# Optimization experiments

Hardware: AMD Instinct MI355X
Metric: run time of the kernel (lower is better)

The kernel has to match this reference:

```python
import jax, jax.numpy as jnp
import numpy as np
import math

D_MODEL, N_HEADS, D_HEAD, D_MLP = 768, 12, 64, 3072
EPS = 1e-5
IGNORE = -100000.0


def _ln(x, w, b):
    mu = jnp.mean(x, axis=-1, keepdims=True)
    xc = x - mu
    scale = jnp.sqrt(jnp.mean(xc * xc, axis=-1, keepdims=True) + EPS)
    return (xc / scale) * w + b


def _gelu_new(x):
    # GPT-2 'new' gelu
    return 0.5 * x * (1.0 + jnp.tanh(jnp.sqrt(2.0 / jnp.pi) * (x + 0.044715 * x ** 3)))


def setup_inputs() -> dict:
    key = jax.random.key(0)
    ks = jax.random.split(key, 12)
    std = 0.02
    inp = {
        "resid_pre": jax.random.normal(ks[0], (8, 1024, D_MODEL), jnp.float32),
        "W_Q": jax.random.normal(ks[1], (N_HEADS, D_MODEL, D_HEAD), jnp.float32) * std,
        "b_Q": jnp.zeros((N_HEADS, D_HEAD), jnp.float32),
        "W_K": jax.random.normal(ks[2], (N_HEADS, D_MODEL, D_HEAD), jnp.float32) * std,
        "b_K": jnp.zeros((N_HEADS, D_HEAD), jnp.float32),
        "W_V": jax.random.normal(ks[3], (N_HEADS, D_MODEL, D_HEAD), jnp.float32) * std,
        "b_V": jnp.zeros((N_HEADS, D_HEAD), jnp.float32),
        "W_O": jax.random.normal(ks[4], (N_HEADS, D_HEAD, D_MODEL), jnp.float32) * std,
        "b_O": jnp.zeros((D_MODEL,), jnp.float32),
        "ln1_w": jnp.ones((D_MODEL,), jnp.float32),
        "ln1_b": jnp.zeros((D_MODEL,), jnp.float32),
        "ln2_w": jnp.ones((D_MODEL,), jnp.float32),
        "ln2_b": jnp.zeros((D_MODEL,), jnp.float32),
        "W_in": jax.random.normal(ks[5], (D_MODEL, D_MLP), jnp.float32) * std,
        "b_in": jnp.zeros((D_MLP,), jnp.float32),
        "W_out": jax.random.normal(ks[6], (D_MLP, D_MODEL), jnp.float32) * std,
        "b_out": jnp.zeros((D_MODEL,), jnp.float32),
    }
    return inp


def reference(resid_pre, W_Q, b_Q, W_K, b_K, W_V, b_V, W_O, b_O,
              ln1_w, ln1_b, ln2_w, ln2_b, W_in, b_in, W_out, b_out):
    # ---- ln1 + attention ----
    n = _ln(resid_pre, ln1_w, ln1_b)  # [b, s, d]; broadcast over heads in einsums
    q = jnp.einsum('bsd,hde->bshe', n, W_Q) + b_Q
    k = jnp.einsum('bsd,hde->bshe', n, W_K) + b_K
    v = jnp.einsum('bsd,hde->bshe', n, W_V) + b_V
    scores = jnp.einsum('bqhe,bkhe->bhqk', q, k) / math.sqrt(D_HEAD)
    S = scores.shape[-1]
    causal = jnp.triu(jnp.ones((S, S), dtype=bool), k=1)
    scores = jnp.where(causal, IGNORE, scores)
    pattern = jax.nn.softmax(scores, axis=-1)
    z = jnp.einsum('bhqk,bkhe->bqhe', pattern, v)
    # per-head output with b_O / n_heads each (as in source), then summed over heads
    attn_per_head = jnp.einsum('bqhe,hed->bqhd', z, W_O) + b_O / N_HEADS
    attn_out = attn_per_head.sum(axis=2)  # [b, s, d]
    resid_mid = resid_pre + attn_out
    # ---- ln2 + mlp ----
    n2 = _ln(resid_mid, ln2_w, ln2_b)
    pre = jnp.einsum('bsd,dm->bsm', n2, W_in) + b_in
    post = _gelu_new(pre)
    mlp_out = jnp.einsum('bsm,md->bsd', post, W_out) + b_out
    return resid_mid + mlp_out
```

## Files before the change

kernel.cpp:

```cpp
#include <hip/hip_runtime.h>
#include <hip/hip_bf16.h>

typedef unsigned short u16;
typedef float f32x4 __attribute__((ext_vector_type(4)));
typedef __bf16 bf16x8 __attribute__((ext_vector_type(8)));
typedef unsigned short u16x8 __attribute__((ext_vector_type(8)));
typedef unsigned short u16x4 __attribute__((ext_vector_type(4)));

__device__ __forceinline__ float b2f(u16 u) {
    unsigned v = ((unsigned)u) << 16;
    return __builtin_bit_cast(float, v);
}
__device__ __forceinline__ u16 f2b(float f) {
    unsigned u = __builtin_bit_cast(unsigned, f);
    u += 0x7fffu + ((u >> 16) & 1u);
    return (u16)(u >> 16);
}
__device__ __forceinline__ bf16x8 ldfrag(const u16* p) {
    return __builtin_bit_cast(bf16x8, *(const u16x8*)p);
}
__device__ __forceinline__ f32x4 mfma16(bf16x8 a, bf16x8 b, f32x4 c) {
    return __builtin_amdgcn_mfma_f32_16x16x32_bf16(a, b, c, 0, 0, 0);
}
__device__ __forceinline__ void gload_lds16(const u16* g, u16* l) {
    __builtin_amdgcn_global_load_lds(
        (const __attribute__((address_space(1))) unsigned int*)(g),
        (__attribute__((address_space(3))) unsigned int*)(l), 16, 0, 0);
}

#define T_TOK 8192
#define DM 768
#define NH 12
#define DH 64
#define DMLP 3072
#define SEQ 1024
#define QKV_LD 2304
#define QK_LD 1536

#define OFF_WQKV ((size_t)0)
#define OFF_WO   (OFF_WQKV + (size_t)2304*768)
#define OFF_WIN  (OFF_WO   + (size_t)768*768)
#define OFF_WOUT (OFF_WIN  + (size_t)768*3072)
#define OFF_BQKV (OFF_WOUT + (size_t)3072*768)
#define P0       (OFF_BQKV + (size_t)4608)

#define SZ_N    ((size_t)T_TOK*DM)
#define SZ_QKV  ((size_t)T_TOK*QKV_LD)
#define A_NBUF   (P0)
#define A_QKV    (P0 + SZ_N)
#define A_Z      (P0 + SZ_N + SZ_QKV)
#define A_N2     (P0)
#define A_POST   (P0 + SZ_N)
#define PATHA_BYTES (((size_t)(P0 + SZ_N + SZ_QKV + SZ_N)) * 2)
#define B_Z      (P0)
#define B_QKVB   (P0 + SZ_N)
#define B_NBUF   (B_QKVB + (size_t)SEQ*QKV_LD)
#define B_N2     (P0)
#define B_POSTC  (P0 + SZ_N)

#define PR0 (2304*768)
#define PR1 (768*768)
#define PR2 (768*3072)
#define PR3 (3072*768)
#define PREP_TOTAL (PR0+PR1+PR2+PR3+2304)

__global__ __launch_bounds__(256) void prep_kernel(
    const float* __restrict__ WQ, const float* __restrict__ WK, const float* __restrict__ WV,
    const float* __restrict__ WO, const float* __restrict__ Win, const float* __restrict__ Wout,
    const float* __restrict__ bQ, const float* __restrict__ bK, const float* __restrict__ bV,
    u16* __restrict__ Wqkv_t, u16* __restrict__ Wo_t, u16* __restrict__ Win_t,
    u16* __restrict__ Wout_t, float* __restrict__ bias_qkv)
{
    int idx = blockIdx.x * 256 + threadIdx.x;
    if (idx < PR0) {
        int r = idx / 768, d = idx % 768;
        int which = r / 768;
        int he = r % 768;
        int h = he >> 6, e = he & 63;
        const float* W = (which == 0) ? WQ : ((which == 1) ? WK : WV);
        Wqkv_t[idx] = f2b(W[h * 49152 + d * 64 + e]);
    } else if (idx < PR0 + PR1) {
        int o = idx - PR0;
        int d = o / 768, he = o % 768;
        Wo_t[o] = f2b(WO[he * 768 + d]);
    } else if (idx < PR0 + PR1 + PR2) {
        int o = idx - PR0 - PR1;
        int m = o / 768, d = o % 768;
        Win_t[o] = f2b(Win[d * 3072 + m]);
    } else if (idx < PR0 + PR1 + PR2 + PR3) {
        int o = idx - PR0 - PR1 - PR2;
        int d = o / 3072, m = o % 3072;
        Wout_t[o] = f2b(Wout[m * 768 + d]);
    } else if (idx < PREP_TOTAL) {
        int j = idx - (PR0 + PR1 + PR2 + PR3);
        bias_qkv[j] = (j < 768) ? bQ[j] : ((j < 1536) ? bK[j - 768] : bV[j - 1536]);
    }
}

__global__ __launch_bounds__(256) void ln_kernel(
    const float* __restrict__ x, const float* __restrict__ w,
    const float* __restrict__ bb, u16* __restrict__ out)
{
    __shared__ float red[4];
    size_t base = (size_t)blockIdx.x * DM;
    int tid = threadIdx.x;
    float v0 = x[base + tid], v1 = x[base + tid + 256], v2 = x[base + tid + 512];
    float s = v0 + v1 + v2;
#pragma unroll
    for (int off = 32; off > 0; off >>= 1) s += __shfl_xor(s, off);
    if ((tid & 63) == 0) red[tid >> 6] = s;
    __syncthreads();
    float mu = (red[0] + red[1] + red[2] + red[3]) * (1.0f / 768.0f);
    v0 -= mu; v1 -= mu; v2 -= mu;
    float q = v0 * v0 + v1 * v1 + v2 * v2;
    __syncthreads();
#pragma unroll
    for (int off = 32; off > 0; off >>= 1) q += __shfl_xor(q, off);
    if ((tid & 63) == 0) red[tid >> 6] = q;
    __syncthreads();
    float var = (red[0] + red[1] + red[2] + red[3]) * (1.0f / 768.0f);
    float sc = rsqrtf(var + 1e-5f);
    out[base + tid]       = f2b(v0 * sc * w[tid]       + bb[tid]);
    out[base + tid + 256] = f2b(v1 * sc * w[tid + 256] + bb[tid + 256]);
    out[base + tid + 512] = f2b(v2 * sc * w[tid + 512] + bb[tid + 512]);
}

template <int EPI, int TM>
__global__ __launch_bounds__(256) void gemm_bt_kernel(
    const u16* __restrict__ A, const u16* __restrict__ BT,
    const float* __restrict__ bias, const float* __restrict__ aux,
    void* __restrict__ outp, int N, int K)
{
    __shared__ __align__(16) u16 As[TM * 32];
    __shared__ __align__(16) u16 Bs[128 * 32];
    const int tid = threadIdx.x;
    const int w = tid >> 6, l = tid & 63;
    const int lr = l & 15, lq = l >> 4;
    const int bm = blockIdx.x * TM, bn = blockIdx.y * 128;
    constexpr int MT = TM / 32;
    const int wm = (w >> 1) * (TM / 2), wn = (w & 1) * 64;

    f32x4 acc[MT][4];
#pragma unroll
    for (int i = 0; i < MT; i++)
#pragma unroll
        for (int j = 0; j < 4; j++) acc[i][j] = f32x4{0.f, 0.f, 0.f, 0.f};

    const int srow_a = (TM == 128) ? (w * 32 + (l >> 2)) : (w * 16 + (l >> 2));
    const int srow_b = w * 32 + (l >> 2);
    const int scol = ((l & 3) ^ ((l >> 2) & 3)) * 8;
    const u16* Ab = A  + (size_t)(bm + srow_a) * K + scol;
    const u16* Bb = BT + (size_t)(bn + srow_b) * K + scol;
    u16* AsD = As + ((TM == 128) ? w * 1024 : w * 512);
    u16* BsD = Bs + w * 1024;
    const int rchunk = (lq ^ (lr & 3)) * 8;

    const int kiter = K >> 5;
    for (int kk = 0; kk < kiter; ++kk) {
        const int k0 = kk * 32;
        gload_lds16(Ab + k0, AsD);
        if (TM == 128) gload_lds16(Ab + 16 * K + k0, AsD + 512);
        gload_lds16(Bb + k0,          BsD);
        gload_lds16(Bb + 16 * K + k0, BsD + 512);
        __syncthreads();
        bf16x8 af[MT], bf[4];
#pragma unroll
        for (int mt = 0; mt < MT; mt++) af[mt] = ldfrag(&As[(wm + mt * 16 + lr) * 32 + rchunk]);
#pragma unroll
        for (int nt = 0; nt < 4; nt++) bf[nt] = ldfrag(&Bs[(wn + nt * 16 + lr) * 32 + rchunk]);
#pragma unroll
        for (int mt = 0; mt < MT; mt++)
#pragma unroll
            for (int nt = 0; nt < 4; nt++)
                acc[mt][nt] = mfma16(af[mt], bf[nt], acc[mt][nt]);
        __syncthreads();
    }

    if (EPI == 4) {
        const bool isv = (bn >= 1536);
        u16* vtg = (u16*)aux;
#pragma unroll
        for (int mt = 0; mt < MT; mt++) {
            int row0 = bm + wm + mt * 16 + lq * 4;
            if (!isv) {
#pragma unroll
                for (int r = 0; r < 4; r++) {
                    size_t ro = (size_t)(row0 + r) * QK_LD;
#pragma unroll
                    for (int nt = 0; nt < 4; nt++) {
                        int col = bn + wn + nt * 16 + lr;
                        ((u16*)outp)[ro + col] = f2b(acc[mt][nt][r] + bias[col]);
                    }
                }
            } else {
                int bloc = row0 >> 10;
                int s = row0 & 1023;
#pragma unroll
                for (int nt = 0; nt < 4; nt++) {
                    int col = bn + wn + nt * 16 + lr;
                    int he = col - 1536;
                    float bcol = bias[col];
                    u16x4 pk;
                    pk[0] = f2b(acc[mt][nt][0] + bcol);
                    pk[1] = f2b(acc[mt][nt][1] + bcol);
                    pk[2] = f2b(acc[mt][nt][2] + bcol);
                    pk[3] = f2b(acc[mt][nt][3] + bcol);
                    *(u16x4*)&vtg[(size_t)bloc * (NH * 64 * SEQ)
                                  + (size_t)he * SEQ + s] = pk;
                }
            }
        }
        return;
    }

#pragma unroll
    for (int mt = 0; mt < MT; mt++) {
#pragma unroll
        for (int r = 0; r < 4; r++) {
            int row = bm + wm + mt * 16 + lq * 4 + r;
            size_t ro = (size_t)row * N;
#pragma unroll
            for (int nt = 0; nt < 4; nt++) {
                int col = bn + wn + nt * 16 + lr;
                float v = acc[mt][nt][r] + bias[col];
                if (EPI == 0) {
                    ((u16*)outp)[ro + col] = f2b(v);
                } else if (EPI == 1) {
                    ((float*)outp)[ro + col] = v + aux[ro + col];
                } else if (EPI == 2) {
                    float x = v;
                    float y = 0.7978845608028654f * (x + 0.044715f * x * x * x);
                    ((u16*)outp)[ro + col] = f2b(x / (1.0f + __expf(-2.0f * y)));
                } else {
                    ((float*)outp)[ro + col] = v + aux[ro + col];
                }
            }
        }
    }
}

__global__ __launch_bounds__(256, 5) void attn_kernel(
    const u16* __restrict__ qk, const u16* __restrict__ vtg,
    u16* __restrict__ z, int b0, int bq0)
{
    __shared__ __align__(16) u16 Ks[64 * 72];
    __shared__ __align__(16) u16 Vt[64 * 72];
    __shared__ __align__(16) u16 Ps[4][16 * 72];

    const int qt = (int)(gridDim.x - 1) - (int)blockIdx.x;
    const int bh = blockIdx.y;
    const int b = b0 + bh / NH, h = bh % NH;
    const int tid = threadIdx.x, w = tid >> 6, l = tid & 63;
    const int lr = l & 15, lq = l >> 4;
    const int qbase = qt * 64;
    const u16* qp = qk + (size_t)(b - bq0) * SEQ * QK_LD + h * 64;
    const u16* kp = qp + 768;
    const u16* vthead = vtg + ((size_t)(b - bq0) * NH + h) * (64 * SEQ);
    u16* PsW = &Ps[w][0];

    bf16x8 aq0, aq1;
    {
        const u16* qrow = qp + (size_t)(qbase + w * 16 + lr) * QK_LD + lq * 8;
        aq0 = ldfrag(qrow);
        aq1 = ldfrag(qrow + 32);
    }

    float m_i = -1e30f;
    float l_i = 0.f;
    f32x4 O[4];
#pragma unroll
    for (int i = 0; i < 4; i++) O[i] = f32x4{0.f, 0.f, 0.f, 0.f};

    const int nkt = qt + 1;
    const int srow = tid >> 2;
    const int spart = (tid & 3) * 16;

    u16x8 kreg0, kreg1, vreg0, vreg1;
    {
        const u16* ks = kp + (size_t)srow * QK_LD + spart;
        kreg0 = *(const u16x8*)ks;
        kreg1 = *(const u16x8*)(ks + 8);
        const u16* vs = vthead + (size_t)srow * SEQ + spart;
        vreg0 = *(const u16x8*)vs;
        vreg1 = *(const u16x8*)(vs + 8);
    }

    for (int kt = 0; kt < nkt; ++kt) {
        __syncthreads();
        *(u16x8*)&Ks[srow * 72 + spart]     = kreg0;
        *(u16x8*)&Ks[srow * 72 + spart + 8] = kreg1;
        *(u16x8*)&Vt[srow * 72 + spart]     = vreg0;
        *(u16x8*)&Vt[srow * 72 + spart + 8] = vreg1;
        __syncthreads();
        if (kt + 1 < nkt) {
            const u16* ks = kp + (size_t)((kt + 1) * 64 + srow) * QK_LD + spart;
            kreg0 = *(const u16x8*)ks;
            kreg1 = *(const u16x8*)(ks + 8);
            const u16* vs = vthead + (size_t)srow * SEQ + (kt + 1) * 64 + spart;
            vreg0 = *(const u16x8*)vs;
            vreg1 = *(const u16x8*)(vs + 8);
        }

        f32x4 S[4];
#pragma unroll
        for (int nt = 0; nt < 4; nt++) S[nt] = f32x4{0.f, 0.f, 0.f, 0.f};
#pragma unroll
        for (int nt = 0; nt < 4; nt++) {
            bf16x8 bk0 = ldfrag(&Ks[(nt * 16 + lr) * 72 + lq * 8]);
            bf16x8 bk1 = ldfrag(&Ks[(nt * 16 + lr) * 72 + 32 + lq * 8]);
            S[nt] = mfma16(bk0, aq0, S[nt]);
            S[nt] = mfma16(bk1, aq1, S[nt]);
        }

        const bool diag = (kt == qt);
        float mx = -1e30f;
#pragma unroll
        for (int nt = 0; nt < 4; nt++)
#pragma unroll
            for (int r = 0; r < 4; r++) {
                float sv = S[nt][r] * 0.125f;
                if (diag) sv = (nt * 16 + lq * 4 + r <= w * 16 + lr) ? sv : -1e30f;
                S[nt][r] = sv;
                mx = fmaxf(mx, sv);
            }
        mx = fmaxf(mx, __shfl_xor(mx, 16));
        mx = fmaxf(mx, __shfl_xor(mx, 32));
        float mn = fmaxf(m_i, mx);
        float alpha = __expf(m_i - mn);
        m_i = mn;
        float rs = 0.f;
#pragma unroll
        for (int nt = 0; nt < 4; nt++) {
            u16x4 pk;
#pragma unroll
            for (int r = 0; r < 4; r++) {
                float pe = __expf(S[nt][r] - mn);
                rs += pe;
                pk[r] = f2b(pe);
            }
            *(u16x4*)&PsW[lr * 72 + nt * 16 + lq * 4] = pk;
        }
        rs += __shfl_xor(rs, 16);
        rs += __shfl_xor(rs, 32);
        l_i = l_i * alpha + rs;

#pragma unroll
        for (int r = 0; r < 4; r++) {
            float ar = __shfl(alpha, (l & 48) | (lq * 4 + r));
            O[0][r] *= ar; O[1][r] *= ar; O[2][r] *= ar; O[3][r] *= ar;
        }

#pragma unroll
        for (int kq = 0; kq < 2; kq++) {
            bf16x8 ap = ldfrag(&PsW[lr * 72 + kq * 32 + lq * 8]);
#pragma unroll
            for (int ot = 0; ot < 4; ot++) {
                bf16x8 bv = ldfrag(&Vt[(ot * 16 + lr) * 72 + kq * 32 + lq * 8]);
                O[ot] = mfma16(ap, bv, O[ot]);
            }
        }
    }

    float li[4];
#pragma unroll
    for (int r = 0; r < 4; r++)
        li[r] = __shfl(l_i, (l & 48) | (lq * 4 + r));
#pragma unroll
    for (int ot = 0; ot < 4; ot++)
#pragma unroll
        for (int r = 0; r < 4; r++) {
            int q = qbase + w * 16 + lq * 4 + r;
            size_t t = (size_t)b * SEQ + q;
            z[t * DM + h * 64 + ot * 16 + lr] = f2b(O[ot][r] / li[r]);
        }
}

extern "C" void kernel_launch(void* const* d_in, const int* in_sizes, int n_in,
                              void* d_out, int out_size, void* d_ws, size_t ws_size,
                              hipStream_t stream) {
    const float* resid_pre = (const float*)d_in[0];
    const float* W_Q  = (const float*)d_in[1];
    const float* b_Q  = (const float*)d_in[2];
    const float* W_K  = (const float*)d_in[3];
    const float* b_K  = (const float*)d_in[4];
    const float* W_V  = (const float*)d_in[5];
    const float* b_V  = (const float*)d_in[6];
    const float* W_O  = (const float*)d_in[7];
    const float* b_O  = (const float*)d_in[8];
    const float* ln1w = (const float*)d_in[9];
    const float* ln1b = (const float*)d_in[10];
    const float* ln2w = (const float*)d_in[11];
    const float* ln2b = (const float*)d_in[12];
    const float* W_in  = (const float*)d_in[13];
    const float* b_in  = (const float*)d_in[14];
    const float* W_out = (const float*)d_in[15];
    const float* b_out = (const float*)d_in[16];

    u16* ws16       = (u16*)d_ws;
    u16* Wqkv_t     = ws16 + OFF_WQKV;
    u16* Wo_t       = ws16 + OFF_WO;
    u16* Win_t      = ws16 + OFF_WIN;
    u16* Wout_t     = ws16 + OFF_WOUT;
    float* bias_qkv = (float*)(ws16 + OFF_BQKV);
    float* outp  = (float*)d_out;
    float* resid = (float*)d_out;

    prep_kernel<<<(PREP_TOTAL + 255) / 256, 256, 0, stream>>>(
        W_Q, W_K, W_V, W_O, W_in, W_out, b_Q, b_K, b_V,
        Wqkv_t, Wo_t, Win_t, Wout_t, bias_qkv);

    if (ws_size >= PATHA_BYTES) {
        u16* nbuf    = ws16 + A_NBUF;
        u16* qkbuf   = ws16 + A_QKV;
        u16* vtgA    = ws16 + A_QKV + (size_t)T_TOK * QK_LD;
        u16* zbuf    = ws16 + A_Z;
        u16* n2buf   = ws16 + A_N2;
        u16* postbuf = ws16 + A_POST;

        ln_kernel<<<T_TOK, 256, 0, stream>>>(resid_pre, ln1w, ln1b, nbuf);
        gemm_bt_kernel<4, 128><<<dim3(T_TOK / 128, QKV_LD / 128), 256, 0, stream>>>(
            nbuf, Wqkv_t, bias_qkv, (const float*)vtgA, qkbuf, QKV_LD, DM);
        attn_kernel<<<dim3(SEQ / 64, 8 * NH), 256, 0, stream>>>(qkbuf, vtgA, zbuf, 0, 0);
        gemm_bt_kernel<1, 64><<<dim3(T_TOK / 64, DM / 128), 256, 0, stream>>>(
            zbuf, Wo_t, b_O, resid_pre, resid, DM, DM);
        ln_kernel<<<T_TOK, 256, 0, stream>>>(resid, ln2w, ln2b, n2buf);
        gemm_bt_kernel<2, 128><<<dim3(T_TOK / 128, DMLP / 128), 256, 0, stream>>>(
            n2buf, Win_t, b_in, nullptr, postbuf, DMLP, DM);
        gemm_bt_kernel<3, 64><<<dim3(T_TOK / 64, DM / 128), 256, 0, stream>>>(
            postbuf, Wout_t, b_out, resid, outp, DM, DMLP);
    } else {
        u16* zbuf   = ws16 + B_Z;
        u16* qkb    = ws16 + B_QKVB;
        u16* vtgB   = qkb + (size_t)SEQ * QK_LD;
        u16* nbuf   = ws16 + B_NBUF;
        u16* n2buf  = ws16 + B_N2;
        u16* postc  = ws16 + B_POSTC;

        ln_kernel<<<T_TOK, 256, 0, stream>>>(resid_pre, ln1w, ln1b, nbuf);
        for (int b = 0; b < 8; b++) {
            gemm_bt_kernel<4, 128><<<dim3(SEQ / 128, QKV_LD / 128), 256, 0, stream>>>(
                nbuf + (size_t)b * SEQ * DM, Wqkv_t, bias_qkv, (const float*)vtgB, qkb, QKV_LD, DM);
            attn_kernel<<<dim3(SEQ / 64, NH), 256, 0, stream>>>(qkb, vtgB, zbuf, b, b);
        }
        gemm_bt_kernel<1, 64><<<dim3(T_TOK / 64, DM / 128), 256, 0, stream>>>(
            zbuf, Wo_t, b_O, resid_pre, resid, DM, DM);
        ln_kernel<<<T_TOK, 256, 0, stream>>>(resid, ln2w, ln2b, n2buf);
        for (int c = 0; c < 4; c++) {
            const size_t r0 = (size_t)c * 2048;
            gemm_bt_kernel<2, 128><<<dim3(2048 / 128, DMLP / 128), 256, 0, stream>>>(
                n2buf + r0 * DM, Win_t, b_in, nullptr, postc, DMLP, DM);
            gemm_bt_kernel<3, 64><<<dim3(2048 / 64, DM / 128), 256, 0, stream>>>(
                postc, Wout_t, b_out, resid + r0 * DM, outp + r0 * DM, DM, DMLP);
        }
    }
}
```

Before: 440.9 us.

## Double-buffer GEMM LDS tiles and vectorize epilogue via transposed MFMA

The GEMM main loop now uses two LDS buffers, issuing the next k-tile's global-to-LDS loads before computing on the current one and dropping one barrier per iteration. For non-QKV epilogues the MFMA operands are swapped so each lane holds four consecutive columns, which lets bias, residual and output be read and written as 4-wide vectors instead of scalars. The XOR swizzle on the LDS layout is removed, which may bring back bank conflicts. LDS use doubles, which can lower occupancy.

```diff
diff --git a/kernel.cpp b/kernel.cpp
--- a/kernel.cpp
+++ b/kernel.cpp
@@ -131,13 +131,14 @@
     const float* __restrict__ bias, const float* __restrict__ aux,
     void* __restrict__ outp, int N, int K)
 {
-    __shared__ __align__(16) u16 As[TM * 32];
-    __shared__ __align__(16) u16 Bs[128 * 32];
+    __shared__ __align__(16) u16 As[2][TM * 32];
+    __shared__ __align__(16) u16 Bs[2][128 * 32];
     const int tid = threadIdx.x;
     const int w = tid >> 6, l = tid & 63;
     const int lr = l & 15, lq = l >> 4;
     const int bm = blockIdx.x * TM, bn = blockIdx.y * 128;
     constexpr int MT = TM / 32;
+    constexpr bool TR = (EPI != 4);
     const int wm = (w >> 1) * (TM / 2), wn = (w & 1) * 64;
 
     f32x4 acc[MT][4];
@@ -148,32 +149,41 @@
 
     const int srow_a = (TM == 128) ? (w * 32 + (l >> 2)) : (w * 16 + (l >> 2));
     const int srow_b = w * 32 + (l >> 2);
-    const int scol = ((l & 3) ^ ((l >> 2) & 3)) * 8;
+    const int scol = (l & 3) * 8;
     const u16* Ab = A  + (size_t)(bm + srow_a) * K + scol;
     const u16* Bb = BT + (size_t)(bn + srow_b) * K + scol;
-    u16* AsD = As + ((TM == 128) ? w * 1024 : w * 512);
-    u16* BsD = Bs + w * 1024;
-    const int rchunk = (lq ^ (lr & 3)) * 8;
+    const int asd = (TM == 128) ? w * 1024 : w * 512;
+    const int bsd = w * 1024;
 
     const int kiter = K >> 5;
+    gload_lds16(Ab, &As[0][asd]);
+    if (TM == 128) gload_lds16(Ab + 16 * K, &As[0][asd + 512]);
+    gload_lds16(Bb, &Bs[0][bsd]);
+    gload_lds16(Bb + 16 * K, &Bs[0][bsd + 512]);
+    __syncthreads();
+
+    int cur = 0;
     for (int kk = 0; kk < kiter; ++kk) {
-        const int k0 = kk * 32;
-        gload_lds16(Ab + k0, AsD);
-        if (TM == 128) gload_lds16(Ab + 16 * K + k0, AsD + 512);
-        gload_lds16(Bb + k0,          BsD);
-        gload_lds16(Bb + 16 * K + k0, BsD + 512);
+        if (kk + 1 < kiter) {
+            const int k0 = (kk + 1) * 32;
+            gload_lds16(Ab + k0, &As[cur ^ 1][asd]);
+            if (TM == 128) gload_lds16(Ab + 16 * K + k0, &As[cur ^ 1][asd + 512]);
+            gload_lds16(Bb + k0,          &Bs[cur ^ 1][bsd]);
+            gload_lds16(Bb + 16 * K + k0, &Bs[cur ^ 1][bsd + 512]);
+        }
+        bf16x8 af[MT], bf[4];
+#pragma unroll
+        for (int mt = 0; mt < MT; mt++) af[mt] = ldfrag(&As[cur][(wm + mt * 16 + lr) * 32 + lq * 8]);
+#pragma unroll
+        for (int nt = 0; nt < 4; nt++) bf[nt] = ldfrag(&Bs[cur][(wn + nt * 16 + lr) * 32 + lq * 8]);
+#pragma unroll
+        for (int mt = 0; mt < MT; mt++)
+#pragma unroll
+            for (int nt = 0; nt < 4; nt++)
+                acc[mt][nt] = TR ? mfma16(bf[nt], af[mt], acc[mt][nt])
+                                 : mfma16(af[mt], bf[nt], acc[mt][nt]);
         __syncthreads();
-        bf16x8 af[MT], bf[4];
-#pragma unroll
-        for (int mt = 0; mt < MT; mt++) af[mt] = ldfrag(&As[(wm + mt * 16 + lr) * 32 + rchunk]);
-#pragma unroll
-        for (int nt = 0; nt < 4; nt++) bf[nt] = ldfrag(&Bs[(wn + nt * 16 + lr) * 32 + rchunk]);
-#pragma unroll
-        for (int mt = 0; mt < MT; mt++)
-#pragma unroll
-            for (int nt = 0; nt < 4; nt++)
-                acc[mt][nt] = mfma16(af[mt], bf[nt], acc[mt][nt]);
-        __syncthreads();
+        cur ^= 1;
     }
 
     if (EPI == 4) {
@@ -215,25 +225,30 @@
 
 #pragma unroll
     for (int mt = 0; mt < MT; mt++) {
-#pragma unroll
-        for (int r = 0; r < 4; r++) {
-            int row = bm + wm + mt * 16 + lq * 4 + r;
-            size_t ro = (size_t)row * N;
-#pragma unroll
-            for (int nt = 0; nt < 4; nt++) {
-                int col = bn + wn + nt * 16 + lr;
-                float v = acc[mt][nt][r] + bias[col];
-                if (EPI == 0) {
-                    ((u16*)outp)[ro + col] = f2b(v);
-                } else if (EPI == 1) {
-                    ((float*)outp)[ro + col] = v + aux[ro + col];
-                } else if (EPI == 2) {
-                    float x = v;
+        int row = bm + wm + mt * 16 + lr;
+        size_t ro = (size_t)row * N;
+#pragma unroll
+        for (int nt = 0; nt < 4; nt++) {
+            int col0 = bn + wn + nt * 16 + lq * 4;
+            f32x4 v = acc[mt][nt] + *(const f32x4*)&bias[col0];
+            if (EPI == 0) {
+                u16x4 pk;
+#pragma unroll
+                for (int r = 0; r < 4; r++) pk[r] = f2b(v[r]);
+                *(u16x4*)&((u16*)outp)[ro + col0] = pk;
+            } else if (EPI == 2) {
+                u16x4 pk;
+#pragma unroll
+                for (int r = 0; r < 4; r++) {
+                    float x = v[r];
                     float y = 0.7978845608028654f * (x + 0.044715f * x * x * x);
-                    ((u16*)outp)[ro + col] = f2b(x / (1.0f + __expf(-2.0f * y)));
-                } else {
-                    ((float*)outp)[ro + col] = v + aux[ro + col];
+                    pk[r] = f2b(x / (1.0f + __expf(-2.0f * y)));
                 }
+                *(u16x4*)&((u16*)outp)[ro + col0] = pk;
+            } else {
+                f32x4 a4 = *(const f32x4*)&aux[ro + col0];
+                v += a4;
+                *(f32x4*)&((float*)outp)[ro + col0] = v;
             }
         }
     }
```

New measurement: 438.0 us. Within noise of the previous version (-0.7%).
